# Performance work log

Hardware: AMD Instinct MI355X
Metric: run time of the kernel (lower is better)

Reference implementation:

```python
import jax, jax.numpy as jnp
import numpy as np

B, S, D, H, V = 4, 1024, 2048, 16, 32000
LAYERS, DFF, HID, NSENT, NLAB = 2, 8192, 100, 3, 3
HD = D // H
LN2 = 0.6931471805599453


def _ln(x, g, b):
    m = jnp.mean(x, axis=-1, keepdims=True)
    v = jnp.mean((x - m) ** 2, axis=-1, keepdims=True)
    return (x - m) * jax.lax.rsqrt(v + 1e-5) * g + b


def setup_inputs():
    key = jax.random.key(0)
    ks = jax.random.split(key, 12)
    s = 0.02
    return dict(
        input_ids=jax.random.randint(ks[0], (B, S), 0, V),
        attention_mask=jnp.ones((B, S), dtype=jnp.int32),
        sentiment=jax.random.normal(ks[1], (B, NSENT), dtype=jnp.float32),
        perplexity=jax.random.uniform(ks[2], (B,), dtype=jnp.float32) + 1.0,
        emb=jax.random.normal(ks[3], (V, D), dtype=jnp.float32) * s,
        ln1_g=jnp.ones((LAYERS, D)), ln1_b=jnp.zeros((LAYERS, D)),
        qkv_w=jax.random.normal(ks[4], (LAYERS, D, 3 * D), dtype=jnp.float32) * s,
        wo_w=jax.random.normal(ks[5], (LAYERS, D, D), dtype=jnp.float32) * s,
        ln2_g=jnp.ones((LAYERS, D)), ln2_b=jnp.zeros((LAYERS, D)),
        w1=jax.random.normal(ks[6], (LAYERS, D, DFF), dtype=jnp.float32) * s,
        w2=jax.random.normal(ks[7], (LAYERS, DFF, D), dtype=jnp.float32) * s,
        lnf_g=jnp.ones((D,)), lnf_b=jnp.zeros((D,)),
        head_w=jax.random.normal(ks[8], (D, V), dtype=jnp.float32) * s,
        red_w=jax.random.normal(ks[9], (D, HID), dtype=jnp.float32) * s,
        red_b=jnp.zeros((HID,)),
        cls_w=jax.random.normal(ks[10], (HID + NSENT + 2, NLAB), dtype=jnp.float32) * s,
        cls_b=jnp.zeros((NLAB,)),
    )


def _lm(input_ids, attention_mask, emb, ln1_g, ln1_b, qkv_w, wo_w, ln2_g, ln2_b, w1, w2, lnf_g, lnf_b, head_w):
    x = emb[input_ids]  # [B,S,D]
    amask = attention_mask.astype(jnp.float32)
    causal = jnp.tril(jnp.ones((S, S), dtype=bool))
    bias = jnp.where(causal[None, None, :, :] & (amask[:, None, None, :] > 0), 0.0, -1e9)
    for l in range(LAYERS):
        h = _ln(x, ln1_g[l], ln1_b[l])
        qkv = h @ qkv_w[l]  # [B,S,3D]
        q, k, v = [t.reshape(B, S, H, HD) for t in jnp.split(qkv, 3, axis=-1)]
        scores = jnp.einsum('bqhd,bkhd->bhqk', q, k) / np.float32(np.sqrt(HD)) + bias
        attn = jax.nn.softmax(scores, axis=-1)
        o = jnp.einsum('bhqk,bkhd->bqhd', attn, v).reshape(B, S, D)
        x = x + o @ wo_w[l]
        h = _ln(x, ln2_g[l], ln2_b[l])
        x = x + jax.nn.gelu(h @ w1[l]) @ w2[l]
    h = _ln(x, lnf_g, lnf_b)
    logits = h @ head_w  # [B,S,V]
    return h, logits


def reference(input_ids, attention_mask, sentiment, perplexity, emb, ln1_g, ln1_b, qkv_w, wo_w, ln2_g, ln2_b, w1, w2, lnf_g, lnf_b, head_w, red_w, red_b, cls_w, cls_b):
    h, logits = _lm(input_ids, attention_mask, emb, ln1_g, ln1_b, qkv_w, wo_w,
                    ln2_g, ln2_b, w1, w2, lnf_g, lnf_b, head_w)
    amask = attention_mask.astype(jnp.float32)
    pooled = jnp.mean(h, axis=1)  # mean over seq -> [B,D]
    # probs = softmax(logits).detach(); gather own token prob; -log2(p)
    lg = jax.lax.stop_gradient(logits)
    logZ = jax.scipy.special.logsumexp(lg, axis=-1)  # [B,S]
    tok_logit = jnp.take_along_axis(lg, input_ids[..., None], axis=-1)[..., 0]
    subword_surp = -(tok_logit - logZ) / LN2 * amask
    mean_surprisal = subword_surp.sum(axis=1) / amask.sum(axis=1)  # [B]
    r = jax.nn.leaky_relu(pooled @ red_w + red_b)  # torch intent: LeakyReLU after reducer
    feats = jnp.concatenate([r, sentiment, perplexity[:, None], mean_surprisal[:, None]], axis=1)
    return feats @ cls_w + cls_b  # [B, NLAB]
```

## Files before the change

kernel.cpp:

```cpp
#include <hip/hip_runtime.h>

typedef unsigned short u16;
typedef __bf16 bf16x8 __attribute__((ext_vector_type(8)));
typedef float f32x4 __attribute__((ext_vector_type(4)));

__device__ __forceinline__ u16 f2bf(float f){
  unsigned u = __float_as_uint(f);
  unsigned r = u + 0x7FFFu + ((u >> 16) & 1u);
  return (u16)(r >> 16);
}
__device__ __forceinline__ float bf2f(u16 v){ return __uint_as_float(((unsigned)v) << 16); }

__device__ __forceinline__ void gload16(const void* g, void* l){
  __builtin_amdgcn_global_load_lds(
      (const __attribute__((address_space(1))) unsigned int*)g,
      (__attribute__((address_space(3))) unsigned int*)l, 16, 0, 0);
}

__global__ __launch_bounds__(256) void transp_k(const float* __restrict__ in, u16* __restrict__ out, int K, int N)
{
  __shared__ float tl[64][65];
  const int n0 = blockIdx.x * 64, k0 = blockIdx.y * 64;
  const int t = threadIdx.x;
  const int r = t >> 4, c4 = t & 15;
#pragma unroll
  for (int i = 0; i < 4; ++i){
    float4 v = *(const float4*)(in + (size_t)(k0 + r + i*16) * N + n0 + c4*4);
    tl[r + i*16][c4*4 + 0] = v.x; tl[r + i*16][c4*4 + 1] = v.y;
    tl[r + i*16][c4*4 + 2] = v.z; tl[r + i*16][c4*4 + 3] = v.w;
  }
  __syncthreads();
#pragma unroll
  for (int i = 0; i < 4; ++i){
    const int n = r + i*16;
    ushort4 o;
    o.x = f2bf(tl[c4*4 + 0][n]); o.y = f2bf(tl[c4*4 + 1][n]);
    o.z = f2bf(tl[c4*4 + 2][n]); o.w = f2bf(tl[c4*4 + 3][n]);
    *(ushort4*)(out + (size_t)(n0 + n) * K + k0 + c4*4) = o;
  }
}

__global__ __launch_bounds__(256) void embed_k(const int* __restrict__ ids, const float* __restrict__ emb, float* __restrict__ x)
{
  const int row = blockIdx.x;
  const int c = blockIdx.y * 256 + threadIdx.x;
  x[(size_t)row * 2048 + c] = emb[(size_t)ids[row] * 2048 + c];
}

__global__ __launch_bounds__(256) void ln_k(const float* __restrict__ x, const float* __restrict__ gw,
                                            const float* __restrict__ bw, u16* __restrict__ o)
{
  const int row = blockIdx.x, t = threadIdx.x;
  const int lane = t & 63, wid = t >> 6;
  const float4* xr = (const float4*)(x + (size_t)row * 2048);
  float4 v1 = xr[t], v2 = xr[t + 256];
  float s1 = v1.x + v1.y + v1.z + v1.w + v2.x + v2.y + v2.z + v2.w;
  float s2 = v1.x*v1.x + v1.y*v1.y + v1.z*v1.z + v1.w*v1.w
           + v2.x*v2.x + v2.y*v2.y + v2.z*v2.z + v2.w*v2.w;
#pragma unroll
  for (int off = 32; off >= 1; off >>= 1){ s1 += __shfl_down(s1, off); s2 += __shfl_down(s2, off); }
  __shared__ float rb[2][4];
  __shared__ float mv[2];
  if (lane == 0){ rb[0][wid] = s1; rb[1][wid] = s2; }
  __syncthreads();
  if (t == 0){
    float a = rb[0][0] + rb[0][1] + rb[0][2] + rb[0][3];
    float q = rb[1][0] + rb[1][1] + rb[1][2] + rb[1][3];
    float mean = a * (1.f/2048.f);
    float var  = q * (1.f/2048.f) - mean*mean;
    mv[0] = mean; mv[1] = rsqrtf(var + 1e-5f);
  }
  __syncthreads();
  const float mean = mv[0], rstd = mv[1];
  const float4* g4 = (const float4*)gw;
  const float4* b4 = (const float4*)bw;
  float4 ga = g4[t], ba = b4[t], gb = g4[t + 256], bb2 = b4[t + 256];
  ushort4 o1, o2;
  o1.x = f2bf((v1.x - mean)*rstd*ga.x + ba.x);
  o1.y = f2bf((v1.y - mean)*rstd*ga.y + ba.y);
  o1.z = f2bf((v1.z - mean)*rstd*ga.z + ba.z);
  o1.w = f2bf((v1.w - mean)*rstd*ga.w + ba.w);
  o2.x = f2bf((v2.x - mean)*rstd*gb.x + bb2.x);
  o2.y = f2bf((v2.y - mean)*rstd*gb.y + bb2.y);
  o2.z = f2bf((v2.z - mean)*rstd*gb.z + bb2.z);
  o2.w = f2bf((v2.w - mean)*rstd*gb.w + bb2.w);
  ((ushort4*)(o + (size_t)row * 2048))[t] = o1;
  ((ushort4*)(o + (size_t)row * 2048))[t + 256] = o2;
}

enum { M_QKV = 0, M_RES = 1, M_GELU = 2, M_LSE = 3 };

template<int MODE>
__global__ __launch_bounds__(512, 4) void gemm7_k(
    const u16* __restrict__ A, const u16* __restrict__ BT,
    int N, int K, int MB,
    u16* __restrict__ outb, float* __restrict__ outf,
    float* __restrict__ partial, float* __restrict__ tokl,
    const int* __restrict__ ids, u16* __restrict__ vtout)
{
  constexpr int ASZ = 128 * 32;
  constexpr int BSZ = 256 * 32;
  constexpr int BUF = ASZ + BSZ;
  __shared__ u16 lds[2 * BUF];

  const int tid  = threadIdx.x;
  const int wv   = tid >> 6, lane = tid & 63;
  const int wr   = wv >> 2,  wc   = wv & 3;
  const int lg   = lane >> 4, lr  = lane & 15;

  const int nwg = gridDim.x;
  const int bid = blockIdx.x;
  const int swz = ((nwg & 7) == 0) ? ((bid & 7) * (nwg >> 3) + (bid >> 3)) : bid;
  const int bm = swz % MB, bn = swz / MB;
  const int m0 = bm * 128, n0 = bn * 256;

  const int ll = lane >> 3;
  const int cc = lane & 7;
  const int lc = cc ^ ll;
  const int gr = (ll << 1) + (lc >> 2);
  const int gk = (lc & 3) << 3;

  const u16* gA = A  + (size_t)m0 * K + gk;
  const u16* gB = BT + (size_t)n0 * K + gk;

  f32x4 acc[4][4];
#pragma unroll
  for (int i = 0; i < 4; ++i)
#pragma unroll
    for (int j = 0; j < 4; ++j)
#pragma unroll
      for (int r = 0; r < 4; ++r) acc[i][j][r] = 0.f;

  const int nt = K >> 5;

  auto STAGE = [&](int bi, int kt){
    char* bA = (char*)lds + (size_t)bi * BUF * 2;
    char* bB = bA + ASZ * 2;
    const size_t ko = (size_t)kt * 32;
    gload16(gA + (size_t)(wv * 16 + gr) * K + ko, bA + wv * 1024);
    gload16(gB + (size_t)((wv    ) * 16 + gr) * K + ko, bB + (wv    ) * 1024);
    gload16(gB + (size_t)((wv + 8) * 16 + gr) * K + ko, bB + (wv + 8) * 1024);
  };

  auto FRAG = [&](const char* base, int row) -> bf16x8 {
    const int p = row >> 1;
    const int slot = (((row & 1) << 2) | lg) ^ (p & 7);
    return *(const bf16x8*)(base + p * 128 + slot * 16);
  };

  STAGE(0, 0);
  STAGE(1, 1);

  for (int t = 0; t < nt; ++t){
    if (t + 1 < nt) asm volatile("s_waitcnt vmcnt(3)" ::: "memory");
    else            asm volatile("s_waitcnt vmcnt(0)" ::: "memory");
    __builtin_amdgcn_s_barrier();

    const char* bA = (const char*)lds + (size_t)(t & 1) * BUF * 2;
    const char* bB = bA + ASZ * 2;
    bf16x8 af[4], bq[4];
#pragma unroll
    for (int i = 0; i < 4; ++i) af[i] = FRAG(bA, wr * 64 + i * 16 + lr);
#pragma unroll
    for (int j = 0; j < 4; ++j) bq[j] = FRAG(bB, wc * 64 + j * 16 + lr);
    asm volatile("s_waitcnt lgkmcnt(0)" ::: "memory");
    __builtin_amdgcn_s_barrier();

    if (t + 2 < nt) STAGE(t & 1, t + 2);

    __builtin_amdgcn_s_setprio(1);
#pragma unroll
    for (int i = 0; i < 4; ++i)
#pragma unroll
      for (int j = 0; j < 4; ++j)
        acc[i][j] = __builtin_amdgcn_mfma_f32_16x16x32_bf16(af[i], bq[j], acc[i][j], 0, 0, 0);
    __builtin_amdgcn_s_setprio(0);
  }

#pragma unroll
  for (int i = 0; i < 4; ++i){
    if constexpr (MODE == M_LSE){
#pragma unroll
      for (int r = 0; r < 4; ++r){
        const int row = m0 + wr * 64 + i * 16 + lg * 4 + r;
        const int id = ids[row];
        float esum = 0.f;
#pragma unroll
        for (int j = 0; j < 4; ++j){
          const int col = n0 + wc * 64 + j * 16 + lr;
          const float v = acc[i][j][r];
          if (col == id) tokl[row] = v;
          esum += __expf(v);
        }
#pragma unroll
        for (int off = 8; off >= 1; off >>= 1) esum += __shfl_xor(esum, off);
        if (lr == 0) partial[(size_t)row * 500 + bn * 4 + wc] = esum;
      }
    } else if constexpr (MODE == M_QKV){
#pragma unroll
      for (int j = 0; j < 4; ++j){
        const int colb = n0 + wc * 64 + j * 16;
        if (colb < 4096){
#pragma unroll
          for (int r = 0; r < 4; ++r){
            const int row = m0 + wr * 64 + i * 16 + lg * 4 + r;
            outb[(size_t)row * 6144 + colb + lr] = f2bf(acc[i][j][r]);
          }
        } else {
          const int srow = m0 + wr * 64 + i * 16 + lg * 4;
          const int b = srow >> 10, s = srow & 1023;
          int dd = colb + lr - 4096;
          const int hh = dd >> 7; dd &= 127;
          ushort4 o;
          o.x = f2bf(acc[i][j][0]); o.y = f2bf(acc[i][j][1]);
          o.z = f2bf(acc[i][j][2]); o.w = f2bf(acc[i][j][3]);
          *(ushort4*)(vtout + ((size_t)(b * 16 + hh) * 128 + dd) * 1024 + s) = o;
        }
      }
    } else {
#pragma unroll
      for (int r = 0; r < 4; ++r){
        const int row = m0 + wr * 64 + i * 16 + lg * 4 + r;
#pragma unroll
        for (int j = 0; j < 4; ++j){
          const int col = n0 + wc * 64 + j * 16 + lr;
          const float v = acc[i][j][r];
          if constexpr (MODE == M_RES){
            float* pp = outf + (size_t)row * N + col;
            *pp += v;
          } else {
            float u = 0.7978845608028654f * (v + 0.044715f * v * v * v);
            u = fminf(fmaxf(u, -15.f), 15.f);
            const float ex = __expf(2.f * u);
            const float th = (ex - 1.f) / (ex + 1.f);
            outb[(size_t)row * N + col] = f2bf(0.5f * v * (1.f + th));
          }
        }
      }
    }
  }
}

__global__ __launch_bounds__(64) void attn_k(const u16* __restrict__ qkv, const u16* __restrict__ vT, u16* __restrict__ o16)
{
  __shared__ u16 P[16 * 40];
  const int bid = blockIdx.x;
  const int qt = bid & 63, bh = bid >> 6;
  const int h = bh & 15, b = bh >> 4;
  const int lane = threadIdx.x, lg = lane >> 4, lr = lane & 15;
  const int q0 = qt << 4;
  const u16* qrow  = qkv + (size_t)(b * 1024 + q0 + lr) * 6144 + h * 128;
  const u16* krow  = qkv + (size_t)(b * 1024 + lr) * 6144 + 2048 + h * 128;
  const u16* vbase = vT + (size_t)(b * 16 + h) * 128 * 1024;

  bf16x8 qf[4];
#pragma unroll
  for (int c = 0; c < 4; ++c) qf[c] = *(const bf16x8*)(qrow + c * 32 + lg * 8);

  float m[4], l[4];
  f32x4 oacc[8];
#pragma unroll
  for (int r = 0; r < 4; ++r){ m[r] = -1e30f; l[r] = 0.f; }
#pragma unroll
  for (int f = 0; f < 8; ++f)
#pragma unroll
    for (int r = 0; r < 4; ++r) oacc[f][r] = 0.f;

  const float scale = 0.08838834764831845f;
  const int nk2 = (qt >> 1) + 1;
  for (int k2 = 0; k2 < nk2; ++k2){
    float e[2][4];
    float rmax[4];
#pragma unroll
    for (int r = 0; r < 4; ++r) rmax[r] = -1e30f;
#pragma unroll
    for (int hh = 0; hh < 2; ++hh){
      const int kt = k2 * 2 + hh;
      if (kt <= qt){
        f32x4 s;
#pragma unroll
        for (int r = 0; r < 4; ++r) s[r] = 0.f;
#pragma unroll
        for (int c = 0; c < 4; ++c){
          bf16x8 kf = *(const bf16x8*)(krow + (size_t)(kt * 16) * 6144 + c * 32 + lg * 8);
          s = __builtin_amdgcn_mfma_f32_16x16x32_bf16(qf[c], kf, s, 0, 0, 0);
        }
#pragma unroll
        for (int r = 0; r < 4; ++r){
          float sv = s[r] * scale;
          if (kt * 16 + lr > q0 + lg * 4 + r) sv = -1e30f;
          e[hh][r] = sv;
          rmax[r] = fmaxf(rmax[r], sv);
        }
      } else {
#pragma unroll
        for (int r = 0; r < 4; ++r) e[hh][r] = -1e30f;
      }
    }
#pragma unroll
    for (int off = 8; off >= 1; off >>= 1)
#pragma unroll
      for (int r = 0; r < 4; ++r) rmax[r] = fmaxf(rmax[r], __shfl_xor(rmax[r], off));
    float corr[4], rsum[4];
#pragma unroll
    for (int r = 0; r < 4; ++r){
      const float mn = fmaxf(m[r], rmax[r]);
      corr[r] = __expf(m[r] - mn);
      m[r] = mn;
      const float e0 = __expf(e[0][r] - mn);
      const float e1 = __expf(e[1][r] - mn);
      e[0][r] = e0; e[1][r] = e1;
      rsum[r] = e0 + e1;
    }
#pragma unroll
    for (int off = 8; off >= 1; off >>= 1)
#pragma unroll
      for (int r = 0; r < 4; ++r) rsum[r] += __shfl_xor(rsum[r], off);
#pragma unroll
    for (int r = 0; r < 4; ++r) l[r] = l[r] * corr[r] + rsum[r];
#pragma unroll
    for (int hh = 0; hh < 2; ++hh)
#pragma unroll
      for (int r = 0; r < 4; ++r)
        P[(lg * 4 + r) * 40 + hh * 16 + lr] = f2bf(e[hh][r]);
#pragma unroll
    for (int f = 0; f < 8; ++f)
#pragma unroll
      for (int r = 0; r < 4; ++r) oacc[f][r] = oacc[f][r] * corr[r];
    __syncthreads();
    const bf16x8 pa = *(const bf16x8*)((const u16*)P + lr * 40 + lg * 8);
#pragma unroll
    for (int f = 0; f < 8; ++f){
      bf16x8 vb = *(const bf16x8*)(vbase + (size_t)(f * 16 + lr) * 1024 + k2 * 32 + lg * 8);
      oacc[f] = __builtin_amdgcn_mfma_f32_16x16x32_bf16(pa, vb, oacc[f], 0, 0, 0);
    }
    __syncthreads();
  }
  u16* orow = o16 + (size_t)(b * 1024 + q0 + lg * 4) * 2048 + h * 128;
#pragma unroll
  for (int r = 0; r < 4; ++r){
    const float linv = 1.0f / l[r];
#pragma unroll
    for (int f = 0; f < 8; ++f)
      orow[(size_t)r * 2048 + f * 16 + lr] = f2bf(oacc[f][r] * linv);
  }
}

__global__ __launch_bounds__(256) void lse_k(const float* __restrict__ partial, const float* __restrict__ tokl,
                                             const int* __restrict__ amask, float* __restrict__ surp)
{
  const int row = blockIdx.x, t = threadIdx.x, lane = t & 63, wid = t >> 6;
  float s = 0.f;
  if (t < 250) s = partial[(size_t)row * 500 + t] + partial[(size_t)row * 500 + t + 250];
#pragma unroll
  for (int off = 32; off >= 1; off >>= 1) s += __shfl_down(s, off);
  __shared__ float rb[4];
  if (lane == 0) rb[wid] = s;
  __syncthreads();
  if (t == 0){
    const float tot = rb[0] + rb[1] + rb[2] + rb[3];
    surp[row] = (logf(tot) - tokl[row]) * 1.4426950408889634f * (float)amask[row];
  }
}

__global__ __launch_bounds__(256) void pool_k(const u16* __restrict__ h16, float* __restrict__ pooled)
{
  const int d = blockIdx.x * 256 + threadIdx.x;
  const int b = blockIdx.y;
  const u16* p = h16 + (size_t)b * 1024 * 2048 + d;
  float a0 = 0.f, a1 = 0.f, a2 = 0.f, a3 = 0.f;
  for (int s = 0; s < 1024; s += 4){
    a0 += bf2f(p[(size_t)(s + 0) * 2048]);
    a1 += bf2f(p[(size_t)(s + 1) * 2048]);
    a2 += bf2f(p[(size_t)(s + 2) * 2048]);
    a3 += bf2f(p[(size_t)(s + 3) * 2048]);
  }
  pooled[b * 2048 + d] = (a0 + a1 + a2 + a3) * (1.f / 1024.f);
}

__global__ __launch_bounds__(256) void cls_k(const float* __restrict__ pooled, const float* __restrict__ surp,
                                             const int* __restrict__ amask, const float* __restrict__ sent,
                                             const float* __restrict__ ppl, const float* __restrict__ redw,
                                             const float* __restrict__ redb, const float* __restrict__ clsw,
                                             const float* __restrict__ clsb, float* __restrict__ out)
{
  const int b = blockIdx.x, t = threadIdx.x;
  const int lane = t & 63, wid = t >> 6;
  __shared__ float pl[2048];
  __shared__ float feats[112];
  __shared__ float rbuf[2][4];
#pragma unroll
  for (int i = 0; i < 8; ++i) pl[t + i * 256] = pooled[b * 2048 + t + i * 256];
  float ssum = 0.f, msum = 0.f;
#pragma unroll
  for (int i = 0; i < 4; ++i){
    const int s = t + i * 256;
    ssum += surp[b * 1024 + s];
    msum += (float)amask[b * 1024 + s];
  }
#pragma unroll
  for (int off = 32; off >= 1; off >>= 1){ ssum += __shfl_down(ssum, off); msum += __shfl_down(msum, off); }
  if (lane == 0){ rbuf[0][wid] = ssum; rbuf[1][wid] = msum; }
  __syncthreads();
  if (t == 0){
    float a = 0.f, c = 0.f;
    for (int i = 0; i < 4; ++i){ a += rbuf[0][i]; c += rbuf[1][i]; }
    feats[104] = a / c;
  }
  if (t >= 100 && t < 103) feats[t] = sent[b * 3 + (t - 100)];
  if (t == 103) feats[103] = ppl[b];
  if (t < 100){
    float a = redb[t];
    for (int d = 0; d < 2048; ++d) a += pl[d] * redw[d * 100 + t];
    feats[t] = (a > 0.f) ? a : 0.01f * a;
  }
  __syncthreads();
  if (t < 3){
    float a = clsb[t];
    for (int i = 0; i < 105; ++i) a += feats[i] * clsw[i * 3 + t];
    out[b * 3 + t] = a;
  }
}

extern "C" void kernel_launch(void* const* d_in, const int* in_sizes, int n_in,
                              void* d_out, int out_size, void* d_ws, size_t ws_size,
                              hipStream_t stream)
{
  (void)in_sizes; (void)n_in; (void)out_size; (void)ws_size;
  const int*   ids   = (const int*)d_in[0];
  const int*   amask = (const int*)d_in[1];
  const float* sent  = (const float*)d_in[2];
  const float* ppl   = (const float*)d_in[3];
  const float* emb   = (const float*)d_in[4];
  const float* ln1g  = (const float*)d_in[5];
  const float* ln1b  = (const float*)d_in[6];
  const float* qkvw  = (const float*)d_in[7];
  const float* wow   = (const float*)d_in[8];
  const float* ln2g  = (const float*)d_in[9];
  const float* ln2b  = (const float*)d_in[10];
  const float* w1    = (const float*)d_in[11];
  const float* w2    = (const float*)d_in[12];
  const float* lnfg  = (const float*)d_in[13];
  const float* lnfb  = (const float*)d_in[14];
  const float* headw = (const float*)d_in[15];
  const float* redw  = (const float*)d_in[16];
  const float* redb  = (const float*)d_in[17];
  const float* clsw  = (const float*)d_in[18];
  const float* clsb  = (const float*)d_in[19];
  float* out = (float*)d_out;

  char* p = (char*)d_ws;
  u16* wqkvT = (u16*)p; p += (size_t)2 * 6144 * 2048 * 2;
  u16* woT   = (u16*)p; p += (size_t)2 * 2048 * 2048 * 2;
  u16* w1T   = (u16*)p; p += (size_t)2 * 8192 * 2048 * 2;
  u16* w2T   = (u16*)p; p += (size_t)2 * 2048 * 8192 * 2;
  u16* whT   = (u16*)p; p += (size_t)32000 * 2048 * 2;
  float* xbuf = (float*)p; p += (size_t)4096 * 2048 * 4;
  u16* h16   = (u16*)p; p += (size_t)4096 * 2048 * 2;
  u16* qkv16 = (u16*)p;
  u16* vT16  = (u16*)(p + (size_t)4096 * 6144 * 2);
  u16* ffn16 = (u16*)p;
  p += (size_t)4096 * 6144 * 2 + (size_t)4096 * 2048 * 2;
  u16* o16   = (u16*)p; p += (size_t)4096 * 2048 * 2;
  float* partial = (float*)p; p += (size_t)4096 * 500 * 4;
  float* tokl = (float*)p; p += (size_t)4096 * 4;
  float* surp = (float*)p; p += (size_t)4096 * 4;
  float* pooled = (float*)p; p += (size_t)4 * 2048 * 4;

  for (int l = 0; l < 2; ++l){
    transp_k<<<dim3(6144/64, 2048/64), 256, 0, stream>>>(qkvw + (size_t)l*2048*6144, wqkvT + (size_t)l*6144*2048, 2048, 6144);
    transp_k<<<dim3(2048/64, 2048/64), 256, 0, stream>>>(wow  + (size_t)l*2048*2048, woT   + (size_t)l*2048*2048, 2048, 2048);
    transp_k<<<dim3(8192/64, 2048/64), 256, 0, stream>>>(w1   + (size_t)l*2048*8192, w1T   + (size_t)l*8192*2048, 2048, 8192);
    transp_k<<<dim3(2048/64, 8192/64), 256, 0, stream>>>(w2   + (size_t)l*8192*2048, w2T   + (size_t)l*2048*8192, 8192, 2048);
  }
  transp_k<<<dim3(32000/64, 2048/64), 256, 0, stream>>>(headw, whT, 2048, 32000);

  embed_k<<<dim3(4096, 8), 256, 0, stream>>>(ids, emb, xbuf);

  for (int l = 0; l < 2; ++l){
    ln_k<<<4096, 256, 0, stream>>>(xbuf, ln1g + l*2048, ln1b + l*2048, h16);
    gemm7_k<M_QKV><<<32*24, 512, 0, stream>>>(h16, wqkvT + (size_t)l*6144*2048, 6144, 2048, 32,
                                              qkv16, nullptr, nullptr, nullptr, nullptr, vT16);
    attn_k<<<4096, 64, 0, stream>>>(qkv16, vT16, o16);
    gemm7_k<M_RES><<<32*8, 512, 0, stream>>>(o16, woT + (size_t)l*2048*2048, 2048, 2048, 32,
                                             nullptr, xbuf, nullptr, nullptr, nullptr, nullptr);
    ln_k<<<4096, 256, 0, stream>>>(xbuf, ln2g + l*2048, ln2b + l*2048, h16);
    gemm7_k<M_GELU><<<32*32, 512, 0, stream>>>(h16, w1T + (size_t)l*8192*2048, 8192, 2048, 32,
                                               ffn16, nullptr, nullptr, nullptr, nullptr, nullptr);
    gemm7_k<M_RES><<<32*8, 512, 0, stream>>>(ffn16, w2T + (size_t)l*2048*8192, 2048, 8192, 32,
                                             nullptr, xbuf, nullptr, nullptr, nullptr, nullptr);
  }
  ln_k<<<4096, 256, 0, stream>>>(xbuf, lnfg, lnfb, h16);
  gemm7_k<M_LSE><<<32*125, 512, 0, stream>>>(h16, whT, 32000, 2048, 32,
                                             nullptr, nullptr, partial, tokl, ids, nullptr);
  lse_k<<<4096, 256, 0, stream>>>(partial, tokl, amask, surp);
  pool_k<<<dim3(8, 4), 256, 0, stream>>>(h16, pooled);
  cls_k<<<4, 256, 0, stream>>>(pooled, surp, amask, sent, ppl, redw, redb, clsw, clsb, out);
}
```

Before: 2.373 ms.

## Run LM-head logsumexp GEMM in FP8 with a larger 256x256 tile

```diff
diff --git a/kernel.cpp b/kernel.cpp
--- a/kernel.cpp
+++ b/kernel.cpp
@@ -1,6 +1,7 @@
 #include <hip/hip_runtime.h>
 
 typedef unsigned short u16;
+typedef unsigned char u8;
 typedef __bf16 bf16x8 __attribute__((ext_vector_type(8)));
 typedef float f32x4 __attribute__((ext_vector_type(4)));
 
@@ -10,6 +11,27 @@
   return (u16)(r >> 16);
 }
 __device__ __forceinline__ float bf2f(u16 v){ return __uint_as_float(((unsigned)v) << 16); }
+
+__device__ __forceinline__ u8 f2fp8(float f){
+  unsigned u = __float_as_uint(f);
+  u8 s = (u >> 24) & 0x80;
+  float a = __uint_as_float(u & 0x7FFFFFFF);
+  if (!(a < 464.f)) return s | 0x7E;
+  unsigned eu = u & 0x7F800000u;
+  unsigned cb = eu + (20u << 23);
+  const unsigned cmin = 141u << 23;
+  float c = __uint_as_float(cb > cmin ? cb : cmin);
+  float q = (a + c) - c;
+  if (q > 448.f) return s | 0x7E;
+  if (q == 0.f) return s;
+  unsigned uq = __float_as_uint(q);
+  int eq = (int)(uq >> 23) - 127;
+  if (eq < -6){
+    int mq = (int)(q * 512.f);
+    return s | (u8)mq;
+  }
+  return s | (u8)(((eq + 7) << 3) | ((uq >> 20) & 7));
+}
 
 __device__ __forceinline__ void gload16(const void* g, void* l){
   __builtin_amdgcn_global_load_lds(
@@ -40,6 +62,29 @@
   }
 }
 
+__global__ __launch_bounds__(256) void transp8_k(const float* __restrict__ in, u8* __restrict__ out, int K, int N)
+{
+  __shared__ float tl[64][65];
+  const int n0 = blockIdx.x * 64, k0 = blockIdx.y * 64;
+  const int t = threadIdx.x;
+  const int r = t >> 4, c4 = t & 15;
+#pragma unroll
+  for (int i = 0; i < 4; ++i){
+    float4 v = *(const float4*)(in + (size_t)(k0 + r + i*16) * N + n0 + c4*4);
+    tl[r + i*16][c4*4 + 0] = v.x; tl[r + i*16][c4*4 + 1] = v.y;
+    tl[r + i*16][c4*4 + 2] = v.z; tl[r + i*16][c4*4 + 3] = v.w;
+  }
+  __syncthreads();
+#pragma unroll
+  for (int i = 0; i < 4; ++i){
+    const int n = r + i*16;
+    uchar4 o;
+    o.x = f2fp8(tl[c4*4 + 0][n] * 16.f); o.y = f2fp8(tl[c4*4 + 1][n] * 16.f);
+    o.z = f2fp8(tl[c4*4 + 2][n] * 16.f); o.w = f2fp8(tl[c4*4 + 3][n] * 16.f);
+    *(uchar4*)(out + (size_t)(n0 + n) * K + k0 + c4*4) = o;
+  }
+}
+
 __global__ __launch_bounds__(256) void embed_k(const int* __restrict__ ids, const float* __restrict__ emb, float* __restrict__ x)
 {
   const int row = blockIdx.x;
@@ -47,8 +92,9 @@
   x[(size_t)row * 2048 + c] = emb[(size_t)ids[row] * 2048 + c];
 }
 
+template<bool FP8>
 __global__ __launch_bounds__(256) void ln_k(const float* __restrict__ x, const float* __restrict__ gw,
-                                            const float* __restrict__ bw, u16* __restrict__ o)
+                                            const float* __restrict__ bw, u16* __restrict__ o, u8* __restrict__ o8)
 {
   const int row = blockIdx.x, t = threadIdx.x;
   const int lane = t & 63, wid = t >> 6;
@@ -75,17 +121,26 @@
   const float4* g4 = (const float4*)gw;
   const float4* b4 = (const float4*)bw;
   float4 ga = g4[t], ba = b4[t], gb = g4[t + 256], bb2 = b4[t + 256];
+  float n1x = (v1.x - mean)*rstd*ga.x + ba.x;
+  float n1y = (v1.y - mean)*rstd*ga.y + ba.y;
+  float n1z = (v1.z - mean)*rstd*ga.z + ba.z;
+  float n1w = (v1.w - mean)*rstd*ga.w + ba.w;
+  float n2x = (v2.x - mean)*rstd*gb.x + bb2.x;
+  float n2y = (v2.y - mean)*rstd*gb.y + bb2.y;
+  float n2z = (v2.z - mean)*rstd*gb.z + bb2.z;
+  float n2w = (v2.w - mean)*rstd*gb.w + bb2.w;
   ushort4 o1, o2;
-  o1.x = f2bf((v1.x - mean)*rstd*ga.x + ba.x);
-  o1.y = f2bf((v1.y - mean)*rstd*ga.y + ba.y);
-  o1.z = f2bf((v1.z - mean)*rstd*ga.z + ba.z);
-  o1.w = f2bf((v1.w - mean)*rstd*ga.w + ba.w);
-  o2.x = f2bf((v2.x - mean)*rstd*gb.x + bb2.x);
-  o2.y = f2bf((v2.y - mean)*rstd*gb.y + bb2.y);
-  o2.z = f2bf((v2.z - mean)*rstd*gb.z + bb2.z);
-  o2.w = f2bf((v2.w - mean)*rstd*gb.w + bb2.w);
+  o1.x = f2bf(n1x); o1.y = f2bf(n1y); o1.z = f2bf(n1z); o1.w = f2bf(n1w);
+  o2.x = f2bf(n2x); o2.y = f2bf(n2y); o2.z = f2bf(n2z); o2.w = f2bf(n2w);
   ((ushort4*)(o + (size_t)row * 2048))[t] = o1;
   ((ushort4*)(o + (size_t)row * 2048))[t + 256] = o2;
+  if constexpr (FP8){
+    uchar4 q1, q2;
+    q1.x = f2fp8(n1x); q1.y = f2fp8(n1y); q1.z = f2fp8(n1z); q1.w = f2fp8(n1w);
+    q2.x = f2fp8(n2x); q2.y = f2fp8(n2y); q2.z = f2fp8(n2z); q2.w = f2fp8(n2w);
+    *(uchar4*)(o8 + (size_t)row * 2048 + t * 4) = q1;
+    *(uchar4*)(o8 + (size_t)row * 2048 + 1024 + t * 4) = q2;
+  }
 }
 
 enum { M_QKV = 0, M_RES = 1, M_GELU = 2, M_LSE = 3 };
@@ -179,24 +234,7 @@
 
 #pragma unroll
   for (int i = 0; i < 4; ++i){
-    if constexpr (MODE == M_LSE){
-#pragma unroll
-      for (int r = 0; r < 4; ++r){
-        const int row = m0 + wr * 64 + i * 16 + lg * 4 + r;
-        const int id = ids[row];
-        float esum = 0.f;
-#pragma unroll
-        for (int j = 0; j < 4; ++j){
-          const int col = n0 + wc * 64 + j * 16 + lr;
-          const float v = acc[i][j][r];
-          if (col == id) tokl[row] = v;
-          esum += __expf(v);
-        }
-#pragma unroll
-        for (int off = 8; off >= 1; off >>= 1) esum += __shfl_xor(esum, off);
-        if (lr == 0) partial[(size_t)row * 500 + bn * 4 + wc] = esum;
-      }
-    } else if constexpr (MODE == M_QKV){
+    if constexpr (MODE == M_QKV){
 #pragma unroll
       for (int j = 0; j < 4; ++j){
         const int colb = n0 + wc * 64 + j * 16;
@@ -237,6 +275,95 @@
           }
         }
       }
+    }
+  }
+}
+
+__global__ __launch_bounds__(512, 2) void gemm8_k(
+    const u8* __restrict__ A8, const u8* __restrict__ B8,
+    int N, int K, int MB,
+    float* __restrict__ partial, float* __restrict__ tokl,
+    const int* __restrict__ ids)
+{
+  __shared__ u8 lds8[2 * 16384];
+
+  const int tid  = threadIdx.x;
+  const int wv   = tid >> 6, lane = tid & 63;
+  const int wr   = wv >> 2,  wc   = wv & 3;
+  const int lg   = lane >> 4, lr  = lane & 15;
+
+  const int nwg = gridDim.x;
+  const int bid = blockIdx.x;
+  const int swz = ((nwg & 7) == 0) ? ((bid & 7) * (nwg >> 3) + (bid >> 3)) : bid;
+  const int bm = swz % MB, bn = swz / MB;
+  const int m0 = bm * 256, n0 = bn * 256;
+
+  const int sr = lane >> 1, sh = (lane & 1) << 4;
+  const u8* gA = A8 + (size_t)(m0 + wv * 32 + sr) * K + sh;
+  const u8* gB = B8 + (size_t)(n0 + wv * 32 + sr) * K + sh;
+
+  f32x4 acc[8][4];
+#pragma unroll
+  for (int i = 0; i < 8; ++i)
+#pragma unroll
+    for (int j = 0; j < 4; ++j)
+#pragma unroll
+      for (int r = 0; r < 4; ++r) acc[i][j][r] = 0.f;
+
+  const int nt = K >> 5;
+
+  auto STAGE = [&](int bi, int kt){
+    u8* base = lds8 + bi * 16384;
+    gload16(gA + (size_t)kt * 32, base + wv * 1024);
+    gload16(gB + (size_t)kt * 32, base + 8192 + wv * 1024);
+  };
+
+  STAGE(0, 0);
+  STAGE(1, 1);
+
+  for (int t = 0; t < nt; ++t){
+    if (t + 1 < nt) asm volatile("s_waitcnt vmcnt(2)" ::: "memory");
+    else            asm volatile("s_waitcnt vmcnt(0)" ::: "memory");
+    __builtin_amdgcn_s_barrier();
+
+    const u8* bA = lds8 + (t & 1) * 16384;
+    const u8* bB = bA + 8192;
+    long af[8], bq[4];
+#pragma unroll
+    for (int i = 0; i < 8; ++i) af[i] = *(const long*)(bA + (wr * 128 + i * 16 + lr) * 32 + lg * 8);
+#pragma unroll
+    for (int j = 0; j < 4; ++j) bq[j] = *(const long*)(bB + (wc * 64 + j * 16 + lr) * 32 + lg * 8);
+    asm volatile("s_waitcnt lgkmcnt(0)" ::: "memory");
+    __builtin_amdgcn_s_barrier();
+
+    if (t + 2 < nt) STAGE(t & 1, t + 2);
+
+    __builtin_amdgcn_s_setprio(1);
+#pragma unroll
+    for (int i = 0; i < 8; ++i)
+#pragma unroll
+      for (int j = 0; j < 4; ++j)
+        acc[i][j] = __builtin_amdgcn_mfma_f32_16x16x32_fp8_fp8(af[i], bq[j], acc[i][j], 0, 0, 0);
+    __builtin_amdgcn_s_setprio(0);
+  }
+
+#pragma unroll
+  for (int i = 0; i < 8; ++i){
+#pragma unroll
+    for (int r = 0; r < 4; ++r){
+      const int row = m0 + wr * 128 + i * 16 + lg * 4 + r;
+      const int id = ids[row];
+      float esum = 0.f;
+#pragma unroll
+      for (int j = 0; j < 4; ++j){
+        const int col = n0 + wc * 64 + j * 16 + lr;
+        const float v = acc[i][j][r] * 0.0625f;
+        if (col == id) tokl[row] = v;
+        esum += __expf(v);
+      }
+#pragma unroll
+      for (int off = 8; off >= 1; off >>= 1) esum += __shfl_xor(esum, off);
+      if (lr == 0) partial[(size_t)row * 500 + bn * 4 + wc] = esum;
     }
   }
 }
@@ -454,9 +581,10 @@
   u16* woT   = (u16*)p; p += (size_t)2 * 2048 * 2048 * 2;
   u16* w1T   = (u16*)p; p += (size_t)2 * 8192 * 2048 * 2;
   u16* w2T   = (u16*)p; p += (size_t)2 * 2048 * 8192 * 2;
-  u16* whT   = (u16*)p; p += (size_t)32000 * 2048 * 2;
+  u8*  wh8   = (u8*)p;  p += (size_t)32000 * 2048;
   float* xbuf = (float*)p; p += (size_t)4096 * 2048 * 4;
   u16* h16   = (u16*)p; p += (size_t)4096 * 2048 * 2;
+  u8*  h8    = (u8*)p;  p += (size_t)4096 * 2048;
   u16* qkv16 = (u16*)p;
   u16* vT16  = (u16*)(p + (size_t)4096 * 6144 * 2);
   u16* ffn16 = (u16*)p;
@@ -473,26 +601,25 @@
     transp_k<<<dim3(8192/64, 2048/64), 256, 0, stream>>>(w1   + (size_t)l*2048*8192, w1T   + (size_t)l*8192*2048, 2048, 8192);
     transp_k<<<dim3(2048/64, 8192/64), 256, 0, stream>>>(w2   + (size_t)l*8192*2048, w2T   + (size_t)l*2048*8192, 8192, 2048);
   }
-  transp_k<<<dim3(32000/64, 2048/64), 256, 0, stream>>>(headw, whT, 2048, 32000);
+  transp8_k<<<dim3(32000/64, 2048/64), 256, 0, stream>>>(headw, wh8, 2048, 32000);
 
   embed_k<<<dim3(4096, 8), 256, 0, stream>>>(ids, emb, xbuf);
 
   for (int l = 0; l < 2; ++l){
-    ln_k<<<4096, 256, 0, stream>>>(xbuf, ln1g + l*2048, ln1b + l*2048, h16);
+    ln_k<false><<<4096, 256, 0, stream>>>(xbuf, ln1g + l*2048, ln1b + l*2048, h16, nullptr);
     gemm7_k<M_QKV><<<32*24, 512, 0, stream>>>(h16, wqkvT + (size_t)l*6144*2048, 6144, 2048, 32,
                                               qkv16, nullptr, nullptr, nullptr, nullptr, vT16);
     attn_k<<<4096, 64, 0, stream>>>(qkv16, vT16, o16);
     gemm7_k<M_RES><<<32*8, 512, 0, stream>>>(o16, woT + (size_t)l*2048*2048, 2048, 2048, 32,
                                              nullptr, xbuf, nullptr, nullptr, nullptr, nullptr);
-    ln_k<<<4096, 256, 0, stream>>>(xbuf, ln2g + l*2048, ln2b + l*2048, h16);
+    ln_k<false><<<4096, 256, 0, stream>>>(xbuf, ln2g + l*2048, ln2b + l*2048, h16, nullptr);
     gemm7_k<M_GELU><<<32*32, 512, 0, stream>>>(h16, w1T + (size_t)l*8192*2048, 8192, 2048, 32,
                                                ffn16, nullptr, nullptr, nullptr, nullptr, nullptr);
     gemm7_k<M_RES><<<32*8, 512, 0, stream>>>(ffn16, w2T + (size_t)l*2048*8192, 2048, 8192, 32,
                                              nullptr, xbuf, nullptr, nullptr, nullptr, nullptr);
   }
-  ln_k<<<4096, 256, 0, stream>>>(xbuf, lnfg, lnfb, h16);
-  gemm7_k<M_LSE><<<32*125, 512, 0, stream>>>(h16, whT, 32000, 2048, 32,
-                                             nullptr, nullptr, partial, tokl, ids, nullptr);
+  ln_k<true><<<4096, 256, 0, stream>>>(xbuf, lnfg, lnfb, h16, h8);
+  gemm8_k<<<16*125, 512, 0, stream>>>(h8, wh8, 32000, 2048, 16, partial, tokl, ids);
   lse_k<<<4096, 256, 0, stream>>>(partial, tokl, amask, surp);
   pool_k<<<dim3(8, 4), 256, 0, stream>>>(h16, pooled);
   cls_k<<<4, 256, 0, stream>>>(pooled, surp, amask, sent, ppl, redw, redb, clsw, clsb, out);
```

Result: slower. 2.544 ms (+7.2%).
